# Performance work log

Hardware: AMD Instinct MI355X
Metric: run time of the kernel (lower is better)

## Reference

```python
import jax, jax.numpy as jnp
import numpy as np

B, N, K = 8, 2048, 32
EPS = 1e-5


def _lrelu(x):
    return jnp.where(x >= 0, x, 0.2 * x)


def _bn(x, p):
    # inference BatchNorm; x: [B, C, ...], p: [4, C] = (gamma, beta, mean, var)
    g, b, m, v = p[0], p[1], p[2], p[3]
    shape = (1, -1) + (1,) * (x.ndim - 2)
    scale = g * jax.lax.rsqrt(v + EPS)
    return (x - m.reshape(shape)) * scale.reshape(shape) + b.reshape(shape)


def _group(x, k):
    # ops.group with xyz_or_feature='feature', feature_or_diff='diff'
    # x: [B, C, N] -> edge features [B, 2C, N, k] = cat(neighbor - center, center)
    xt = jnp.transpose(x, (0, 2, 1))  # [B, N, C]
    sq = jnp.sum(xt * xt, axis=-1)    # [B, N]
    dist = sq[:, :, None] - 2.0 * jnp.einsum('bnc,bmc->bnm', xt, xt) + sq[:, None, :]
    idx = jax.lax.top_k(-dist, k)[1]  # [B, N, k] nearest neighbors
    nbr = jax.vmap(lambda f, i: f[i])(xt, idx)  # [B, N, k, C]
    center = xt[:, :, None, :]
    edge = jnp.concatenate([nbr - center, jnp.broadcast_to(center, nbr.shape)], axis=-1)
    return jnp.transpose(edge, (0, 3, 1, 2))  # [B, 2C, N, k]


def _edgeconv(x, w1, bn1, w2, bn2, k):
    e = _group(x, k)
    h = _lrelu(_bn(jnp.einsum('oc,bcnk->bonk', w1, e), bn1))
    h = _lrelu(_bn(jnp.einsum('oc,bcnk->bonk', w2, h), bn2))
    return jnp.max(h, axis=-1)  # max over neighbors -> [B, C_out, N]


def _model(x,
           ec1_w1, ec1_bn1, ec1_w2, ec1_bn2,
           ec2_w1, ec2_bn1, ec2_w2, ec2_bn2,
           ec3_w1, ec3_bn1, ec3_w2, ec3_bn2,
           emb_w, q_w, k_w, v_w, att_bn1, ff_w1, ff_w2, att_bn2,
           cb_w, cb_bn):
    # EdgeConvBlock (3 stacked EdgeConvs, outputs concatenated)
    f1 = _edgeconv(x, ec1_w1, ec1_bn1, ec1_w2, ec1_bn2, K)
    f2 = _edgeconv(f1, ec2_w1, ec2_bn1, ec2_w2, ec2_bn2, K)
    f3 = _edgeconv(f2, ec3_w1, ec3_bn1, ec3_w2, ec3_bn2, K)
    xc = jnp.concatenate([f1, f2, f3], axis=1)  # [B, 192, N]
    # Point2PointAttentionBlock: embedding then dense self-attention
    h = jnp.einsum('oc,bcn->bon', emb_w, xc)  # [B, 1024, N]
    q = jnp.einsum('oc,bcn->bon', q_w, h)
    kk = jnp.einsum('oc,bcn->bon', k_w, h)
    v = jnp.einsum('oc,bcn->bon', v_w, h)
    scale = jnp.sqrt(jnp.asarray(h.shape[1], h.dtype))
    att = jax.nn.softmax(jnp.einsum('bcn,bcm->bnm', q, kk) / scale, axis=-1)  # [B, N, N]
    x_r = jnp.einsum('bnm,bcm->bcn', att, v)
    h = _bn(h + x_r, att_bn1)
    ff = jnp.einsum('oc,bcn->bon', ff_w2, _lrelu(jnp.einsum('oc,bcn->bon', ff_w1, h)))
    h = _bn(h + ff, att_bn2)
    # ConvBlock head
    return _lrelu(_bn(jnp.einsum('oc,bcn->bon', cb_w, h), cb_bn))  # [B, 1024, N]


def setup_inputs() -> dict:
    key = jax.random.key(0)
    ks = iter(jax.random.split(key, 32))

    def randn(shape, s=0.1):
        return jax.random.normal(next(ks), shape, jnp.float32) * s

    def bnp(c):
        return jax.random.uniform(next(ks), (4, c), jnp.float32, 0.1, 1.0)

    return {
        'x': randn((B, 3, N), 1.0),
        'ec1_w1': randn((64, 6)), 'ec1_bn1': bnp(64),
        'ec1_w2': randn((64, 64)), 'ec1_bn2': bnp(64),
        'ec2_w1': randn((64, 128)), 'ec2_bn1': bnp(64),
        'ec2_w2': randn((64, 64)), 'ec2_bn2': bnp(64),
        'ec3_w1': randn((64, 128)), 'ec3_bn1': bnp(64),
        'ec3_w2': randn((64, 64)), 'ec3_bn2': bnp(64),
        'emb_w': randn((1024, 192), 0.05),
        'q_w': randn((1024, 1024), 0.03),
        'k_w': randn((1024, 1024), 0.03),
        'v_w': randn((1024, 1024), 0.03),
        'att_bn1': bnp(1024),
        'ff_w1': randn((512, 1024), 0.03),
        'ff_w2': randn((1024, 512), 0.03),
        'att_bn2': bnp(1024),
        'cb_w': randn((1024, 1024), 0.03),
        'cb_bn': bnp(1024),
    }


def reference(x,
              ec1_w1, ec1_bn1, ec1_w2, ec1_bn2,
              ec2_w1, ec2_bn1, ec2_w2, ec2_bn2,
              ec3_w1, ec3_bn1, ec3_w2, ec3_bn2,
              emb_w, q_w, k_w, v_w, att_bn1, ff_w1, ff_w2, att_bn2,
              cb_w, cb_bn):
    return _model(x,
                  ec1_w1, ec1_bn1, ec1_w2, ec1_bn2,
                  ec2_w1, ec2_bn1, ec2_w2, ec2_bn2,
                  ec3_w1, ec3_bn1, ec3_w2, ec3_bn2,
                  emb_w, q_w, k_w, v_w, att_bn1, ff_w1, ff_w2, att_bn2,
                  cb_w, cb_bn)
```

## Files before the change

kernel.cpp:

```cpp
#include <hip/hip_runtime.h>
#include <hip/hip_bf16.h>

constexpr int Bn  = 8;
constexpr int Np  = 2048;
constexpr int KNN = 32;

typedef __attribute__((ext_vector_type(8))) short bf16x8;
typedef __attribute__((ext_vector_type(4))) float f32x4;

__device__ static inline void gll16(const void* g, void* l) {
  __builtin_amdgcn_global_load_lds((const __attribute__((address_space(1))) void*)g,
                                   (__attribute__((address_space(3))) void*)l, 16, 0, 0);
}

__device__ static inline unsigned short f2bf(float x) {
  union { __hip_bfloat16 h; unsigned short u; } cv; cv.h = __float2bfloat16(x); return cv.u;
}
__device__ static inline float bf2f(unsigned short u) {
  union { __hip_bfloat16 h; unsigned short u; } cv; cv.u = u; return __bfloat162float(cv.h);
}

__global__ __launch_bounds__(256)
void cvt_bf16_kernel(const float* __restrict__ s, __hip_bfloat16* __restrict__ d, int n) {
  int i = blockIdx.x * 256 + threadIdx.x;
  if (i < n) d[i] = __float2bfloat16(s[i]);
}

template<int CIN, int K1>
__global__ __launch_bounds__(256)
void cvt_w1a(const float* __restrict__ w1, __hip_bfloat16* __restrict__ out) {
  int i = blockIdx.x * 256 + threadIdx.x;
  if (i >= 64 * K1) return;
  int o = i / K1, c = i - o * K1;
  out[i] = __float2bfloat16(c < CIN ? w1[o * 2 * CIN + c] : 0.f);
}

__global__ __launch_bounds__(256)
void xpose_kernel(const float* __restrict__ x, float* __restrict__ xt,
                  __hip_bfloat16* __restrict__ xb) {
  int i = blockIdx.x * 256 + threadIdx.x;
  int b = i >> 11, n = i & 2047;
  const float* p = x + (long)b * 3 * Np + n;
  float vx = p[0], vy = p[Np], vz = p[2 * Np];
  xt[(long)i * 4 + 0] = vx;
  xt[(long)i * 4 + 1] = vy;
  xt[(long)i * 4 + 2] = vz;
  xt[(long)i * 4 + 3] = 0.f;
  __hip_bfloat16* q = xb + (long)i * 8;
  q[0] = __float2bfloat16(vx); q[1] = __float2bfloat16(vy);
  q[2] = __float2bfloat16(vz);
  q[3] = __float2bfloat16(0.f); q[4] = q[3]; q[5] = q[3]; q[6] = q[3]; q[7] = q[3];
}

template<int C, int CP>
__global__ __launch_bounds__(256)
void sq_kernel(const float* __restrict__ f, float* __restrict__ out) {
  int i = blockIdx.x * 256 + threadIdx.x;
  const float* p = f + (long)i * CP;
  float s = 0.f;
#pragma unroll
  for (int c = 0; c < C; ++c) s += p[c] * p[c];
  out[i] = s;
}

template<int CIN, int CP>
__global__ __launch_bounds__(256)
void split_kernel(const float* __restrict__ f, __hip_bfloat16* __restrict__ fhi,
                  __hip_bfloat16* __restrict__ flo) {
  int i = blockIdx.x * 256 + threadIdx.x;
  int n = i >> 6, c = i & 63;
  float v = (c < CIN) ? f[(long)n * CP + c] : 0.f;
  __hip_bfloat16 h = __float2bfloat16(v);
  fhi[i] = h;
  flo[i] = __float2bfloat16(v - __bfloat162float(h));
}

__device__ static inline unsigned umin32(unsigned a, unsigned b) { return a < b ? a : b; }

__device__ static inline unsigned long long shfl64x(unsigned long long k, int m) {
  unsigned lo = (unsigned)__shfl_xor((int)(unsigned)k, m);
  unsigned hi = (unsigned)__shfl_xor((int)(unsigned)(k >> 32), m);
  return ((unsigned long long)hi << 32) | (unsigned long long)lo;
}

__device__ static inline unsigned lane_sort64_u32(unsigned v, int lane) {
#pragma unroll
  for (int k = 2; k <= 64; k <<= 1) {
#pragma unroll
    for (int j = k >> 1; j > 0; j >>= 1) {
      unsigned o = (unsigned)__shfl_xor((int)v, j);
      bool dir = ((lane & k) == 0);
      bool lower = ((lane & j) == 0);
      bool keep = (v < o) == (dir == lower);
      v = keep ? v : o;
    }
  }
  return v;
}

__device__ static inline unsigned long long lane_sort64_u64(unsigned long long v, int lane) {
#pragma unroll
  for (int k = 2; k <= 64; k <<= 1) {
#pragma unroll
    for (int j = k >> 1; j > 0; j >>= 1) {
      unsigned long long o = shfl64x(v, j);
      bool dir = ((lane & k) == 0);
      bool lower = ((lane & j) == 0);
      bool keep = (v < o) == (dir == lower);
      v = keep ? v : o;
    }
  }
  return v;
}

__device__ static inline unsigned long long lane_merge64(unsigned long long a,
                                                         unsigned long long b, int lane) {
  unsigned long long br = shfl64x(b, 63);
  unsigned long long m = a < br ? a : br;
#pragma unroll
  for (int j = 32; j > 0; j >>= 1) {
    unsigned long long o = shfl64x(m, j);
    bool lower = ((lane & j) == 0);
    bool keep = (m < o) == lower;
    m = keep ? m : o;
  }
  return m;
}

template<int MAP>
__device__ static inline void row_topk(const unsigned* val, unsigned long long* cbuf,
                                       int lane, int* outp) {
  unsigned tmn[16];
#pragma unroll
  for (int i = 0; i < 16; ++i) tmn[i] = umin32(val[i], val[i + 16]);
#pragma unroll
  for (int w2 = 8; w2 >= 1; w2 >>= 1)
#pragma unroll
    for (int i = 0; i < 8; ++i)
      if (i < w2) tmn[i] = umin32(tmn[i], tmn[i + w2]);

  unsigned T = (unsigned)__shfl((int)lane_sort64_u32(tmn[0], lane), 31);

  int S = 0;
#pragma unroll
  for (int s = 0; s < 32; ++s) {
    bool p = val[s] <= T;
    unsigned long long mask = __ballot(p);
    int pre = __builtin_amdgcn_mbcnt_hi((unsigned)(mask >> 32),
              __builtin_amdgcn_mbcnt_lo((unsigned)mask, 0u));
    int pos = S + pre;
    unsigned idx = (MAP == 0) ? (unsigned)((s >> 2) * 256 + lane * 4 + (s & 3))
                              : (unsigned)((s >> 2) * 256 + (s & 3) * 64 + lane);
    if (p && pos < 256) cbuf[pos] = ((unsigned long long)val[s] << 32) | idx;
    S += (int)__popcll(mask);
  }

  unsigned long long cur;
  if (S <= 256) {
    unsigned long long k0 = (lane < S) ? cbuf[lane] : ~0ull;
    cur = lane_sort64_u64(k0, lane);
    for (int c = 64; c < S; c += 64) {
      unsigned long long kc = (c + lane < S) ? cbuf[c + lane] : ~0ull;
      cur = lane_merge64(cur, lane_sort64_u64(kc, lane), lane);
    }
  } else {
    cur = ~0ull;
    for (int s = 0; s < 32; ++s) {
      unsigned idx = (MAP == 0) ? (unsigned)((s >> 2) * 256 + lane * 4 + (s & 3))
                                : (unsigned)((s >> 2) * 256 + (s & 3) * 64 + lane);
      unsigned long long kc = ((unsigned long long)val[s] << 32) | idx;
      cur = lane_merge64(cur, lane_sort64_u64(kc, lane), lane);
    }
  }
  if (lane < KNN) outp[lane] = (int)(unsigned)cur;
}

__global__ __launch_bounds__(512)
void knn3_kernel(const float* __restrict__ xt, const float* __restrict__ sqb,
                 int* __restrict__ idxOut) {
  __shared__ float4 F[2048];
  __shared__ float sqS[2048];
  __shared__ unsigned long long cbuf[8 * 256];
  int t = threadIdx.x, lane = t & 63, w = t >> 6;
  long pb = (long)blockIdx.y * Np;
  for (int e = t; e < 2048; e += 512) {
    F[e] = ((const float4*)xt)[pb + e];
    sqS[e] = sqb[pb + e];
  }
  __syncthreads();
  int row = blockIdx.x * 8 + w;
  float4 a = F[row];
  unsigned val[32];
#pragma unroll
  for (int j4 = 0; j4 < 8; ++j4)
#pragma unroll
    for (int u = 0; u < 4; ++u) {
      int col = j4 * 256 + u * 64 + lane;
      float4 fb = F[col];
      float d = sqS[col] - 2.f * (a.x * fb.x + a.y * fb.y + a.z * fb.z);
      unsigned b = __float_as_uint(d);
      val[j4 * 4 + u] = b ^ ((unsigned)((int)b >> 31) | 0x80000000u);
    }
  row_topk<1>(val, cbuf + w * 256, lane, idxOut + (pb + row) * KNN);
}

__global__ __launch_bounds__(512)
void knn16_kernel(const __hip_bfloat16* __restrict__ fhi,
                  const __hip_bfloat16* __restrict__ flo,
                  const float* __restrict__ sqb, int* __restrict__ idxOut) {
  constexpr int LDW = 2052;
  __shared__ __align__(16) float Dw[16 * LDW];
  __shared__ float sqS[2048];
  __shared__ unsigned long long cbuf[8 * 256];
  int t = threadIdx.x, lane = t & 63, w = t >> 6;
  long pb = (long)blockIdx.y * Np;
  int r0 = blockIdx.x * 16;
  const __hip_bfloat16* fh = fhi + pb * 64;
  const __hip_bfloat16* fl = flo + pb * 64;

  ((float4*)sqS)[t] = ((const float4*)(sqb + pb))[t];

  int ar = r0 + (lane & 15);
  int kc = (lane >> 4) * 8;
  bf16x8 ah[2], al[2];
#pragma unroll
  for (int k2 = 0; k2 < 2; ++k2) {
    ah[k2] = *(const bf16x8*)(fh + (long)ar * 64 + k2 * 32 + kc);
    al[k2] = *(const bf16x8*)(fl + (long)ar * 64 + k2 * 32 + kc);
  }
  __syncthreads();

  int cb0 = w * 256;
  bf16x8 bh[2], bl[2];
  {
    int bcol = cb0 + (lane & 15);
#pragma unroll
    for (int k2 = 0; k2 < 2; ++k2) {
      bh[k2] = *(const bf16x8*)(fh + (long)bcol * 64 + k2 * 32 + kc);
      bl[k2] = *(const bf16x8*)(fl + (long)bcol * 64 + k2 * 32 + kc);
    }
  }
  for (int ct = 0; ct < 16; ++ct) {
    bf16x8 nh[2], nl[2];
    if (ct < 15) {
      int bcol = cb0 + (ct + 1) * 16 + (lane & 15);
#pragma unroll
      for (int k2 = 0; k2 < 2; ++k2) {
        nh[k2] = *(const bf16x8*)(fh + (long)bcol * 64 + k2 * 32 + kc);
        nl[k2] = *(const bf16x8*)(fl + (long)bcol * 64 + k2 * 32 + kc);
      }
    }
    f32x4 acc = f32x4{0.f, 0.f, 0.f, 0.f};
#pragma unroll
    for (int k2 = 0; k2 < 2; ++k2) {
      acc = __builtin_amdgcn_mfma_f32_16x16x32_bf16(ah[k2], bh[k2], acc, 0, 0, 0);
      acc = __builtin_amdgcn_mfma_f32_16x16x32_bf16(ah[k2], bl[k2], acc, 0, 0, 0);
      acc = __builtin_amdgcn_mfma_f32_16x16x32_bf16(al[k2], bh[k2], acc, 0, 0, 0);
    }
    int col0 = cb0 + ct * 16;
    int n = lane & 15, m0 = (lane >> 4) * 4;
    float sqv = sqS[col0 + n];
#pragma unroll
    for (int r = 0; r < 4; ++r)
      Dw[(m0 + r) * LDW + col0 + n] = sqv - 2.f * acc[r];
#pragma unroll
    for (int k2 = 0; k2 < 2; ++k2) { bh[k2] = nh[k2]; bl[k2] = nl[k2]; }
  }
  __syncthreads();

  for (int rr = 0; rr < 2; ++rr) {
    int row = w * 2 + rr;
    unsigned val[32];
    const float4* rp = (const float4*)&Dw[row * LDW];
#pragma unroll
    for (int j4 = 0; j4 < 8; ++j4) {
      float4 f4 = rp[j4 * 64 + lane];
      float fv[4] = {f4.x, f4.y, f4.z, f4.w};
#pragma unroll
      for (int u = 0; u < 4; ++u) {
        unsigned b = __float_as_uint(fv[u]);
        val[j4 * 4 + u] = b ^ ((unsigned)((int)b >> 31) | 0x80000000u);
      }
    }
    row_topk<0>(val, cbuf + w * 256, lane, idxOut + (pb + r0 + row) * KNN);
  }
}

template<int CIN, int CP>
__global__ __launch_bounds__(256)
void biasker(const float* __restrict__ feat, const float* __restrict__ w1,
             float* __restrict__ bias) {
  __shared__ float wd[64][CIN + 1];
  int tid = threadIdx.x;
  for (int e = tid; e < 64 * CIN; e += 256) {
    int o = e / CIN, c = e - o * CIN;
    wd[o][c] = w1[o * 2 * CIN + CIN + c] - w1[o * 2 * CIN + c];
  }
  __syncthreads();
  int wv = tid >> 6, o = tid & 63;
  float wr_[CIN];
#pragma unroll
  for (int c = 0; c < CIN; ++c) wr_[c] = wd[o][c];
  long base = (long)blockIdx.y * Np + blockIdx.x * 32 + wv * 8;
  for (int p = 0; p < 8; ++p) {
    const float* fr = feat + (base + p) * CP;
    float acc = 0.f;
#pragma unroll
    for (int c = 0; c < CIN; ++c) acc = fmaf(wr_[c], fr[c], acc);
    bias[(base + p) * 64 + o] = acc;
  }
}

template<int K1>
__global__ __launch_bounds__(256)
void edge_mfma(const __hip_bfloat16* __restrict__ featb, int fstride,
               const int* __restrict__ idx, const float* __restrict__ bias,
               const __hip_bfloat16* __restrict__ w1b,
               const __hip_bfloat16* __restrict__ w2b,
               const float* __restrict__ bn1, const float* __restrict__ bn2,
               float* __restrict__ fout, __hip_bfloat16* __restrict__ xcseg) {
  __shared__ __align__(16) char lds[32768 + 64 * K1 * 2 + 8192 + 1024 + 512];
  __hip_bfloat16* A  = (__hip_bfloat16*)lds;
  __hip_bfloat16* H1 = A + 128 * K1;
  float*          H2 = (float*)lds;
  __hip_bfloat16* W1 = (__hip_bfloat16*)(lds + 32768);
  __hip_bfloat16* W2 = W1 + 64 * K1;
  float* biasS = (float*)(lds + 32768 + 64 * K1 * 2 + 8192);
  int*   idxS  = (int*)(biasS + 256);

  int t = threadIdx.x, lane = t & 63, w = t >> 6;
  long pb = (long)blockIdx.y * Np;
  int p0 = blockIdx.x * 4;

  if (t < 128) idxS[t] = idx[(pb + p0 + (t >> 5)) * KNN + (t & 31)];
  biasS[w * 64 + lane] = bias[(pb + p0 + w) * 64 + lane];
  for (int e = t; e < 64 * K1 / 8; e += 256)
    ((ulonglong2*)W1)[e] = ((const ulonglong2*)w1b)[e];
  for (int e = t; e < 512; e += 256)
    ((ulonglong2*)W2)[e] = ((const ulonglong2*)w2b)[e];
  __syncthreads();

  if (K1 == 64) {
#pragma unroll
    for (int i = 0; i < 4; ++i) {
      int e = t + i * 256;
      int r = e >> 3, cc = e & 7;
      const ulonglong2* src = (const ulonglong2*)(featb + (pb + idxS[r]) * fstride) + cc;
      ((ulonglong2*)(A + r * 64))[cc] = *src;
    }
  } else {
    if (t < 128) {
      int r = t;
      ulonglong2 z; z.x = 0; z.y = 0;
      ((ulonglong2*)(A + r * 32))[0] = *(const ulonglong2*)(featb + (pb + idxS[r]) * fstride);
      ((ulonglong2*)(A + r * 32))[1] = z;
      ((ulonglong2*)(A + r * 32))[2] = z;
      ((ulonglong2*)(A + r * 32))[3] = z;
    }
  }

  int ocol = lane & 15;
  float sc1[4], sh1[4], sc2[4], sh2[4];
#pragma unroll
  for (int jn = 0; jn < 4; ++jn) {
    int o = jn * 16 + ocol;
    sc1[jn] = bn1[o] * rsqrtf(bn1[192 + o] + 1e-5f);
    sh1[jn] = bn1[64 + o] - bn1[128 + o] * sc1[jn];
    sc2[jn] = bn2[o] * rsqrtf(bn2[192 + o] + 1e-5f);
    sh2[jn] = bn2[64 + o] - bn2[128 + o] * sc2[jn];
  }
  __syncthreads();

  int mrow = lane & 15;
  int kc   = (lane >> 4) * 8;
  constexpr int KS = K1 / 32;

  f32x4 acc[2][4];
#pragma unroll
  for (int im = 0; im < 2; ++im)
#pragma unroll
    for (int jn = 0; jn < 4; ++jn) acc[im][jn] = f32x4{0.f, 0.f, 0.f, 0.f};
#pragma unroll
  for (int s = 0; s < KS; ++s) {
    bf16x8 af[2], bf_[4];
#pragma unroll
    for (int im = 0; im < 2; ++im)
      af[im] = *(const bf16x8*)(A + (w * 32 + im * 16 + mrow) * K1 + s * 32 + kc);
#pragma unroll
    for (int jn = 0; jn < 4; ++jn)
      bf_[jn] = *(const bf16x8*)(W1 + (jn * 16 + mrow) * K1 + s * 32 + kc);
#pragma unroll
    for (int im = 0; im < 2; ++im)
#pragma unroll
      for (int jn = 0; jn < 4; ++jn)
        acc[im][jn] = __builtin_amdgcn_mfma_f32_16x16x32_bf16(af[im], bf_[jn], acc[im][jn], 0, 0, 0);
  }
#pragma unroll
  for (int im = 0; im < 2; ++im)
#pragma unroll
    for (int jn = 0; jn < 4; ++jn) {
      int o = jn * 16 + ocol;
      float bsv = biasS[w * 64 + o];
#pragma unroll
      for (int r = 0; r < 4; ++r) {
        int m = w * 32 + im * 16 + (lane >> 4) * 4 + r;
        float x = (acc[im][jn][r] + bsv) * sc1[jn] + sh1[jn];
        x = fmaxf(x, 0.2f * x);
        H1[m * 64 + o] = __float2bfloat16(x);
      }
    }
  __syncthreads();

  bf16x8 a2[2][2], b2[4][2];
#pragma unroll
  for (int im = 0; im < 2; ++im)
#pragma unroll
    for (int s = 0; s < 2; ++s)
      a2[im][s] = *(const bf16x8*)(H1 + (w * 32 + im * 16 + mrow) * 64 + s * 32 + kc);
#pragma unroll
  for (int jn = 0; jn < 4; ++jn)
#pragma unroll
    for (int s = 0; s < 2; ++s)
      b2[jn][s] = *(const bf16x8*)(W2 + (jn * 16 + mrow) * 64 + s * 32 + kc);
  __syncthreads();

  f32x4 acc2[2][4];
#pragma unroll
  for (int im = 0; im < 2; ++im)
#pragma unroll
    for (int jn = 0; jn < 4; ++jn) acc2[im][jn] = f32x4{0.f, 0.f, 0.f, 0.f};
#pragma unroll
  for (int s = 0; s < 2; ++s)
#pragma unroll
    for (int im = 0; im < 2; ++im)
#pragma unroll
      for (int jn = 0; jn < 4; ++jn)
        acc2[im][jn] = __builtin_amdgcn_mfma_f32_16x16x32_bf16(a2[im][s], b2[jn][s], acc2[im][jn], 0, 0, 0);
#pragma unroll
  for (int im = 0; im < 2; ++im)
#pragma unroll
    for (int jn = 0; jn < 4; ++jn) {
      int o = jn * 16 + ocol;
#pragma unroll
      for (int r = 0; r < 4; ++r) {
        int m = w * 32 + im * 16 + (lane >> 4) * 4 + r;
        float x = acc2[im][jn][r] * sc2[jn] + sh2[jn];
        x = fmaxf(x, 0.2f * x);
        H2[m * 64 + o] = x;
      }
    }
  __syncthreads();

  {
    int o = t & 63;
    float m = -3.4e38f;
#pragma unroll
    for (int k = 0; k < 32; ++k) m = fmaxf(m, H2[(w * 32 + k) * 64 + o]);
    int n2 = p0 + w;
    if (fout) fout[(pb + n2) * 64 + o] = m;
    xcseg[(pb + n2) * 192 + o] = __float2bfloat16(m);
  }
}

template<int OUTF, int BNMODE, int RESID, int LRELU>
__global__ __launch_bounds__(512)
void gemm_db(const __hip_bfloat16* __restrict__ A, int lda, long sA,
             const __hip_bfloat16* __restrict__ B, int ldb, long sB,
             void* __restrict__ Cv, int ldc, long sC,
             const __hip_bfloat16* __restrict__ R, long sR,
             const float* __restrict__ bn, int bnlen, int Kd,
             int gx, int gy) {
  int nwg = gx * gy * Bn;
  int cpx = nwg >> 3;
  int orig = blockIdx.x;
  int wg = (orig & 7) * cpx + (orig >> 3);
  int bz = wg / (gx * gy);
  int rem = wg - bz * (gx * gy);
  int by = rem / gx;
  int bx = rem - by * gx;
  A += (long)bz * sA;
  B += (long)bz * sB;
  long i0 = (long)bx * 256, j0 = (long)by * 256;

  __shared__ __hip_bfloat16 As[2][256 * 64];
  __shared__ __hip_bfloat16 Bs[2][256 * 64];

  int t = threadIdx.x, lane = t & 63, w = t >> 6;
  int wm = w & 1, wn = w >> 1;

  f32x4 acc[8][4];
#pragma unroll
  for (int im = 0; im < 8; ++im)
#pragma unroll
    for (int jn = 0; jn < 4; ++jn) acc[im][jn] = f32x4{0.f, 0.f, 0.f, 0.f};

#define STAGE_DB(bi, kt)                                                     \
  {                                                                          \
    _Pragma("unroll")                                                        \
    for (int i = 0; i < 4; ++i) {                                            \
      int e = t + i * 512;                                                   \
      int r = e >> 3, c = e & 7;                                             \
      int cs = c ^ (r & 7);                                                  \
      gll16(A + (i0 + r) * lda + (kt) * 64 + cs * 8,                         \
            (__hip_bfloat16*)As[bi] + e * 8);                                \
    }                                                                        \
    _Pragma("unroll")                                                        \
    for (int i = 0; i < 4; ++i) {                                            \
      int e = t + i * 512;                                                   \
      int r = e >> 3, c = e & 7;                                             \
      int cs = c ^ (r & 7);                                                  \
      gll16(B + (j0 + r) * ldb + (kt) * 64 + cs * 8,                         \
            (__hip_bfloat16*)Bs[bi] + e * 8);                                \
    }                                                                        \
  }

  int nt = Kd >> 6;
  STAGE_DB(0, 0);
  __syncthreads();

  int cur = 0;
  for (int kt = 0; kt < nt; ++kt) {
    if (kt + 1 < nt) STAGE_DB(cur ^ 1, kt + 1);
    const __hip_bfloat16* Ab = As[cur];
    const __hip_bfloat16* Bb = Bs[cur];
#pragma unroll
    for (int ks = 0; ks < 2; ++ks) {
      bf16x8 af[8], bfv[4];
#pragma unroll
      for (int im = 0; im < 8; ++im) {
        int ra = wm * 128 + im * 16 + (lane & 15);
        int q = (ks * 4 + (lane >> 4)) ^ (ra & 7);
        af[im] = *(const bf16x8*)(Ab + ra * 64 + q * 8);
      }
#pragma unroll
      for (int jn = 0; jn < 4; ++jn) {
        int rb = wn * 64 + jn * 16 + (lane & 15);
        int q = (ks * 4 + (lane >> 4)) ^ (rb & 7);
        bfv[jn] = *(const bf16x8*)(Bb + rb * 64 + q * 8);
      }
#pragma unroll
      for (int im = 0; im < 8; ++im)
#pragma unroll
        for (int jn = 0; jn < 4; ++jn)
          acc[im][jn] = __builtin_amdgcn_mfma_f32_16x16x32_bf16(af[im], bfv[jn], acc[im][jn], 0, 0, 0);
    }
    __syncthreads();
    cur ^= 1;
  }
#undef STAGE_DB

  int mlocal = (lane >> 4) * 4;
  int nlocal = lane & 15;
#pragma unroll
  for (int i = 0; i < 8; ++i) {
    long m0 = i0 + wm * 128 + i * 16 + mlocal;
    float bsc[4], bsh[4];
    if (BNMODE == 1) {
#pragma unroll
      for (int r = 0; r < 4; ++r) {
        long c = m0 + r;
        float sc = bn[c] * rsqrtf(bn[3 * bnlen + c] + 1e-5f);
        bsc[r] = sc;
        bsh[r] = bn[bnlen + c] - bn[2 * bnlen + c] * sc;
      }
    }
#pragma unroll
    for (int j = 0; j < 4; ++j) {
      long nn = j0 + wn * 64 + j * 16 + nlocal;
      float sc2 = 1.f, sh2 = 0.f;
      if (BNMODE == 2) {
        sc2 = bn[nn] * rsqrtf(bn[3 * bnlen + nn] + 1e-5f);
        sh2 = bn[bnlen + nn] - bn[2 * bnlen + nn] * sc2;
      }
      f32x4 v = acc[i][j];
      float o4[4];
      ushort4 rv;
      if (RESID) rv = *(const ushort4*)(R + (long)bz * sR + nn * ldc + m0);
#pragma unroll
      for (int r = 0; r < 4; ++r) {
        float x = v[r];
        if (RESID) x += bf2f(r == 0 ? rv.x : r == 1 ? rv.y : r == 2 ? rv.z : rv.w);
        if (BNMODE == 1) x = x * bsc[r] + bsh[r];
        if (BNMODE == 2) x = x * sc2 + sh2;
        if (LRELU) x = (x >= 0.f) ? x : 0.2f * x;
        o4[r] = x;
      }
      if (OUTF) {
        float* Cp = (float*)Cv + (long)bz * sC + nn * ldc + m0;
        *(float4*)Cp = make_float4(o4[0], o4[1], o4[2], o4[3]);
      } else {
        __hip_bfloat16* Cp = (__hip_bfloat16*)Cv + (long)bz * sC + nn * ldc + m0;
        ushort4 sv;
        sv.x = f2bf(o4[0]); sv.y = f2bf(o4[1]); sv.z = f2bf(o4[2]); sv.w = f2bf(o4[3]);
        *(ushort4*)Cp = sv;
      }
    }
  }
}

__global__ __launch_bounds__(256)
void softmax_bf(__hip_bfloat16* __restrict__ S) {
  long row = (long)blockIdx.y * Np + blockIdx.x;
  __hip_bfloat16* p = S + row * Np;
  int t = threadIdx.x;
  const float scale = 0.03125f;
  float v[8];
  float mx = -3.4e38f;
#pragma unroll
  for (int u = 0; u < 8; ++u) {
    v[u] = __bfloat162float(p[u * 256 + t]) * scale;
    mx = fmaxf(mx, v[u]);
  }
  __shared__ float red[4];
#pragma unroll
  for (int off = 32; off > 0; off >>= 1) mx = fmaxf(mx, __shfl_xor(mx, off));
  if ((t & 63) == 0) red[t >> 6] = mx;
  __syncthreads();
  mx = fmaxf(fmaxf(red[0], red[1]), fmaxf(red[2], red[3]));
  __syncthreads();
  float sum = 0.f;
#pragma unroll
  for (int u = 0; u < 8; ++u) { v[u] = __expf(v[u] - mx); sum += v[u]; }
#pragma unroll
  for (int off = 32; off > 0; off >>= 1) sum += __shfl_xor(sum, off);
  if ((t & 63) == 0) red[t >> 6] = sum;
  __syncthreads();
  sum = red[0] + red[1] + red[2] + red[3];
  float inv = 1.f / sum;
#pragma unroll
  for (int u = 0; u < 8; ++u) p[u * 256 + t] = __float2bfloat16(v[u] * inv);
}

extern "C" void kernel_launch(void* const* d_in, const int* in_sizes, int n_in,
                              void* d_out, int out_size, void* d_ws, size_t ws_size,
                              hipStream_t stream) {
  const float* x       = (const float*)d_in[0];
  const float* ec1_w1  = (const float*)d_in[1];
  const float* ec1_bn1 = (const float*)d_in[2];
  const float* ec1_w2  = (const float*)d_in[3];
  const float* ec1_bn2 = (const float*)d_in[4];
  const float* ec2_w1  = (const float*)d_in[5];
  const float* ec2_bn1 = (const float*)d_in[6];
  const float* ec2_w2  = (const float*)d_in[7];
  const float* ec2_bn2 = (const float*)d_in[8];
  const float* ec3_w1  = (const float*)d_in[9];
  const float* ec3_bn1 = (const float*)d_in[10];
  const float* ec3_w2  = (const float*)d_in[11];
  const float* ec3_bn2 = (const float*)d_in[12];
  const float* emb_w   = (const float*)d_in[13];
  const float* q_w     = (const float*)d_in[14];
  const float* k_w     = (const float*)d_in[15];
  const float* v_w     = (const float*)d_in[16];
  const float* att_bn1 = (const float*)d_in[17];
  const float* ff_w1   = (const float*)d_in[18];
  const float* ff_w2   = (const float*)d_in[19];
  const float* att_bn2 = (const float*)d_in[20];
  const float* cb_w    = (const float*)d_in[21];
  const float* cb_bn   = (const float*)d_in[22];
  float* out = (float*)d_out;
  (void)in_sizes; (void)n_in; (void)out_size; (void)ws_size;

  float* ws  = (float*)d_ws;
  float* xt  = ws;
  float* f1  = xt + 65536;
  float* f2  = f1 + 1048576;
  float* sqb = f2 + 1048576;
  int*   idxb = (int*)(sqb + 16384);
  __hip_bfloat16* xc  = (__hip_bfloat16*)(idxb + 524288);
  __hip_bfloat16* wts = xc + 3145728;
  __hip_bfloat16* ew  = wts + 5439488;
  __hip_bfloat16* xb  = ew + 22528;
  float* big = (float*)(xb + 131072);
  __hip_bfloat16* hb  = (__hip_bfloat16*)big;
  __hip_bfloat16* qb  = hb + 16777216;
  __hip_bfloat16* kb  = qb + 16777216;
  __hip_bfloat16* vtb = kb + 16777216;
  __hip_bfloat16* Sb  = vtb + 16777216;
  __hip_bfloat16* fhi = (__hip_bfloat16*)big;
  __hip_bfloat16* flo = fhi + 1048576;
  float* biasb = big + 33554432;

  __hip_bfloat16* emb_wb = wts;
  __hip_bfloat16* q_wb   = wts + 196608;
  __hip_bfloat16* k_wb   = wts + 1245184;
  __hip_bfloat16* v_wb   = wts + 2293760;
  __hip_bfloat16* ff1_wb = wts + 3342336;
  __hip_bfloat16* ff2_wb = wts + 3866624;
  __hip_bfloat16* cb_wb  = wts + 4390912;

  __hip_bfloat16* w1a1_b = ew;
  __hip_bfloat16* w2_1b  = ew + 2048;
  __hip_bfloat16* w1a2_b = ew + 6144;
  __hip_bfloat16* w2_2b  = ew + 10240;
  __hip_bfloat16* w1a3_b = ew + 14336;
  __hip_bfloat16* w2_3b  = ew + 18432;

  const long sN1024 = (long)Np * 1024;
  const long sN512  = (long)Np * 512;
  const long sN192  = (long)Np * 192;
  const long sNN    = (long)Np * Np;

  cvt_bf16_kernel<<<768,  256, 0, stream>>>(emb_w, emb_wb, 196608);
  cvt_bf16_kernel<<<4096, 256, 0, stream>>>(q_w,   q_wb,   1048576);
  cvt_bf16_kernel<<<4096, 256, 0, stream>>>(k_w,   k_wb,   1048576);
  cvt_bf16_kernel<<<4096, 256, 0, stream>>>(v_w,   v_wb,   1048576);
  cvt_bf16_kernel<<<2048, 256, 0, stream>>>(ff_w1, ff1_wb, 524288);
  cvt_bf16_kernel<<<2048, 256, 0, stream>>>(ff_w2, ff2_wb, 524288);
  cvt_bf16_kernel<<<4096, 256, 0, stream>>>(cb_w,  cb_wb,  1048576);
  cvt_w1a<3, 32><<<8, 256, 0, stream>>>(ec1_w1, w1a1_b);
  cvt_w1a<64, 64><<<16, 256, 0, stream>>>(ec2_w1, w1a2_b);
  cvt_w1a<64, 64><<<16, 256, 0, stream>>>(ec3_w1, w1a3_b);
  cvt_bf16_kernel<<<16, 256, 0, stream>>>(ec1_w2, w2_1b, 4096);
  cvt_bf16_kernel<<<16, 256, 0, stream>>>(ec2_w2, w2_2b, 4096);
  cvt_bf16_kernel<<<16, 256, 0, stream>>>(ec3_w2, w2_3b, 4096);

  xpose_kernel<<<64, 256, 0, stream>>>(x, xt, xb);

  sq_kernel<3, 4><<<64, 256, 0, stream>>>(xt, sqb);
  knn3_kernel<<<dim3(Np / 8, Bn), 512, 0, stream>>>(xt, sqb, idxb);
  biasker<3, 4><<<dim3(Np / 32, Bn), 256, 0, stream>>>(xt, ec1_w1, biasb);
  edge_mfma<32><<<dim3(Np / 4, Bn), 256, 0, stream>>>(
      xb, 8, idxb, biasb, w1a1_b, w2_1b, ec1_bn1, ec1_bn2, f1, xc);

  sq_kernel<64, 64><<<64, 256, 0, stream>>>(f1, sqb);
  split_kernel<64, 64><<<4096, 256, 0, stream>>>(f1, fhi, flo);
  knn16_kernel<<<dim3(Np / 16, Bn), 512, 0, stream>>>(fhi, flo, sqb, idxb);
  biasker<64, 64><<<dim3(Np / 32, Bn), 256, 0, stream>>>(f1, ec2_w1, biasb);
  edge_mfma<64><<<dim3(Np / 4, Bn), 256, 0, stream>>>(
      xc, 192, idxb, biasb, w1a2_b, w2_2b, ec2_bn1, ec2_bn2, f2, xc + 64);

  sq_kernel<64, 64><<<64, 256, 0, stream>>>(f2, sqb);
  split_kernel<64, 64><<<4096, 256, 0, stream>>>(f2, fhi, flo);
  knn16_kernel<<<dim3(Np / 16, Bn), 512, 0, stream>>>(fhi, flo, sqb, idxb);
  biasker<64, 64><<<dim3(Np / 32, Bn), 256, 0, stream>>>(f2, ec3_w1, biasb);
  edge_mfma<64><<<dim3(Np / 4, Bn), 256, 0, stream>>>(
      xc + 64, 192, idxb, biasb, w1a3_b, w2_3b, ec3_bn1, ec3_bn2, nullptr, xc + 128);

  gemm_db<0, 0, 0, 0><<<dim3(4 * 8 * Bn), 512, 0, stream>>>(
      emb_wb, 192, 0, xc, 192, sN192, hb, 1024, sN1024, nullptr, 0, nullptr, 0, 192, 4, 8);

  gemm_db<0, 0, 0, 0><<<dim3(4 * 8 * Bn), 512, 0, stream>>>(
      q_wb, 1024, 0, hb, 1024, sN1024, qb, 1024, sN1024, nullptr, 0, nullptr, 0, 1024, 4, 8);
  gemm_db<0, 0, 0, 0><<<dim3(4 * 8 * Bn), 512, 0, stream>>>(
      k_wb, 1024, 0, hb, 1024, sN1024, kb, 1024, sN1024, nullptr, 0, nullptr, 0, 1024, 4, 8);
  gemm_db<0, 0, 0, 0><<<dim3(8 * 4 * Bn), 512, 0, stream>>>(
      hb, 1024, sN1024, v_wb, 1024, 0, vtb, 2048, sN1024, nullptr, 0, nullptr, 0, 1024, 8, 4);

  gemm_db<0, 0, 0, 0><<<dim3(8 * 8 * Bn), 512, 0, stream>>>(
      kb, 1024, sN1024, qb, 1024, sN1024, Sb, 2048, sNN, nullptr, 0, nullptr, 0, 1024, 8, 8);
  softmax_bf<<<dim3(Np, Bn), 256, 0, stream>>>(Sb);

  gemm_db<0, 1, 1, 0><<<dim3(4 * 8 * Bn), 512, 0, stream>>>(
      vtb, 2048, sN1024, Sb, 2048, sNN, hb, 1024, sN1024, hb, sN1024, att_bn1, 1024, 2048, 4, 8);

  gemm_db<0, 0, 0, 1><<<dim3(2 * 8 * Bn), 512, 0, stream>>>(
      ff1_wb, 1024, 0, hb, 1024, sN1024, qb, 512, sN512, nullptr, 0, nullptr, 0, 1024, 2, 8);
  gemm_db<0, 1, 1, 0><<<dim3(4 * 8 * Bn), 512, 0, stream>>>(
      ff2_wb, 512, 0, qb, 512, sN512, hb, 1024, sN1024, hb, sN1024, att_bn2, 1024, 512, 4, 8);

  gemm_db<1, 2, 0, 1><<<dim3(8 * 4 * Bn), 512, 0, stream>>>(
      hb, 1024, sN1024, cb_wb, 1024, 0, out, 2048, sN1024, nullptr, 0, cb_bn, 1024, 1024, 8, 4);
}
```

Before: 952.6 us.

## Shrink knn16 tile to 8 rows to cut LDS and raise occupancy

The 64-channel kNN kernel now handles 8 query rows per block instead of 16. That shrinks the distance tile in shared memory, drops the staged squared-norm array in favour of direct global loads, and caps the candidate buffer at 224 entries. Two column-tile streams are interleaved with software prefetch, and launch bounds ask for 4 blocks per CU. The MFMA still computes 16 rows, so half of each product is wasted work, and B-operand loads are repeated across twice as many blocks. A row with more than 224 candidates now takes the slower full-merge path more often.

```diff
diff --git a/kernel.cpp b/kernel.cpp
--- a/kernel.cpp
+++ b/kernel.cpp
@@ -127,7 +127,7 @@
   return m;
 }
 
-template<int MAP>
+template<int MAP, int CAP>
 __device__ static inline void row_topk(const unsigned* val, unsigned long long* cbuf,
                                        int lane, int* outp) {
   unsigned tmn[16];
@@ -151,12 +151,12 @@
     int pos = S + pre;
     unsigned idx = (MAP == 0) ? (unsigned)((s >> 2) * 256 + lane * 4 + (s & 3))
                               : (unsigned)((s >> 2) * 256 + (s & 3) * 64 + lane);
-    if (p && pos < 256) cbuf[pos] = ((unsigned long long)val[s] << 32) | idx;
+    if (p && pos < CAP) cbuf[pos] = ((unsigned long long)val[s] << 32) | idx;
     S += (int)__popcll(mask);
   }
 
   unsigned long long cur;
-  if (S <= 256) {
+  if (S <= CAP) {
     unsigned long long k0 = (lane < S) ? cbuf[lane] : ~0ull;
     cur = lane_sort64_u64(k0, lane);
     for (int c = 64; c < S; c += 64) {
@@ -201,77 +201,121 @@
       unsigned b = __float_as_uint(d);
       val[j4 * 4 + u] = b ^ ((unsigned)((int)b >> 31) | 0x80000000u);
     }
-  row_topk<1>(val, cbuf + w * 256, lane, idxOut + (pb + row) * KNN);
-}
-
-__global__ __launch_bounds__(512)
+  row_topk<1, 256>(val, cbuf + w * 256, lane, idxOut + (pb + row) * KNN);
+}
+
+__global__ __launch_bounds__(512, 4)
 void knn16_kernel(const __hip_bfloat16* __restrict__ fhi,
                   const __hip_bfloat16* __restrict__ flo,
                   const float* __restrict__ sqb, int* __restrict__ idxOut) {
   constexpr int LDW = 2052;
-  __shared__ __align__(16) float Dw[16 * LDW];
-  __shared__ float sqS[2048];
-  __shared__ unsigned long long cbuf[8 * 256];
+  constexpr int CAP = 224;
+  __shared__ __align__(16) float Dw[8 * LDW];
+  __shared__ unsigned long long cbuf[8 * CAP];
   int t = threadIdx.x, lane = t & 63, w = t >> 6;
   long pb = (long)blockIdx.y * Np;
-  int r0 = blockIdx.x * 16;
+  int r0 = blockIdx.x * 8;
   const __hip_bfloat16* fh = fhi + pb * 64;
   const __hip_bfloat16* fl = flo + pb * 64;
-
-  ((float4*)sqS)[t] = ((const float4*)(sqb + pb))[t];
-
-  int ar = r0 + (lane & 15);
+  const float* sqg = sqb + pb;
+
+  int ar = r0 + (lane & 7);
   int kc = (lane >> 4) * 8;
+  int n15 = lane & 15;
   bf16x8 ah[2], al[2];
 #pragma unroll
   for (int k2 = 0; k2 < 2; ++k2) {
     ah[k2] = *(const bf16x8*)(fh + (long)ar * 64 + k2 * 32 + kc);
     al[k2] = *(const bf16x8*)(fl + (long)ar * 64 + k2 * 32 + kc);
   }
-  __syncthreads();
 
   int cb0 = w * 256;
-  bf16x8 bh[2], bl[2];
+  bf16x8 b0h[2], b0l[2], b1h[2], b1l[2];
+  float sq0, sq1;
   {
-    int bcol = cb0 + (lane & 15);
+    int bc = cb0 + n15;
 #pragma unroll
     for (int k2 = 0; k2 < 2; ++k2) {
-      bh[k2] = *(const bf16x8*)(fh + (long)bcol * 64 + k2 * 32 + kc);
-      bl[k2] = *(const bf16x8*)(fl + (long)bcol * 64 + k2 * 32 + kc);
-    }
-  }
-  for (int ct = 0; ct < 16; ++ct) {
-    bf16x8 nh[2], nl[2];
-    if (ct < 15) {
-      int bcol = cb0 + (ct + 1) * 16 + (lane & 15);
+      b0h[k2] = *(const bf16x8*)(fh + (long)bc * 64 + k2 * 32 + kc);
+      b0l[k2] = *(const bf16x8*)(fl + (long)bc * 64 + k2 * 32 + kc);
+    }
+    sq0 = sqg[bc];
+    bc = cb0 + 16 + n15;
+#pragma unroll
+    for (int k2 = 0; k2 < 2; ++k2) {
+      b1h[k2] = *(const bf16x8*)(fh + (long)bc * 64 + k2 * 32 + kc);
+      b1l[k2] = *(const bf16x8*)(fl + (long)bc * 64 + k2 * 32 + kc);
+    }
+    sq1 = sqg[bc];
+  }
+  int m0 = (lane >> 4) * 4;
+  bool wr = (lane < 32);
+#pragma unroll
+  for (int cp = 0; cp < 8; ++cp) {
+    {
+      int ct = cp * 2;
+      bf16x8 nh[2], nl[2]; float nsq = 0.f;
+      if (ct + 2 < 16) {
+        int bc = cb0 + (ct + 2) * 16 + n15;
+#pragma unroll
+        for (int k2 = 0; k2 < 2; ++k2) {
+          nh[k2] = *(const bf16x8*)(fh + (long)bc * 64 + k2 * 32 + kc);
+          nl[k2] = *(const bf16x8*)(fl + (long)bc * 64 + k2 * 32 + kc);
+        }
+        nsq = sqg[bc];
+      }
+      f32x4 acc = f32x4{0.f, 0.f, 0.f, 0.f};
 #pragma unroll
       for (int k2 = 0; k2 < 2; ++k2) {
-        nh[k2] = *(const bf16x8*)(fh + (long)bcol * 64 + k2 * 32 + kc);
-        nl[k2] = *(const bf16x8*)(fl + (long)bcol * 64 + k2 * 32 + kc);
-      }
-    }
-    f32x4 acc = f32x4{0.f, 0.f, 0.f, 0.f};
-#pragma unroll
-    for (int k2 = 0; k2 < 2; ++k2) {
-      acc = __builtin_amdgcn_mfma_f32_16x16x32_bf16(ah[k2], bh[k2], acc, 0, 0, 0);
-      acc = __builtin_amdgcn_mfma_f32_16x16x32_bf16(ah[k2], bl[k2], acc, 0, 0, 0);
-      acc = __builtin_amdgcn_mfma_f32_16x16x32_bf16(al[k2], bh[k2], acc, 0, 0, 0);
-    }
-    int col0 = cb0 + ct * 16;
-    int n = lane & 15, m0 = (lane >> 4) * 4;
-    float sqv = sqS[col0 + n];
-#pragma unroll
-    for (int r = 0; r < 4; ++r)
-      Dw[(m0 + r) * LDW + col0 + n] = sqv - 2.f * acc[r];
-#pragma unroll
-    for (int k2 = 0; k2 < 2; ++k2) { bh[k2] = nh[k2]; bl[k2] = nl[k2]; }
-  }
-  __syncthreads();
-
-  for (int rr = 0; rr < 2; ++rr) {
-    int row = w * 2 + rr;
+        acc = __builtin_amdgcn_mfma_f32_16x16x32_bf16(ah[k2], b0h[k2], acc, 0, 0, 0);
+        acc = __builtin_amdgcn_mfma_f32_16x16x32_bf16(ah[k2], b0l[k2], acc, 0, 0, 0);
+        acc = __builtin_amdgcn_mfma_f32_16x16x32_bf16(al[k2], b0h[k2], acc, 0, 0, 0);
+      }
+      if (wr) {
+        int col = cb0 + ct * 16 + n15;
+#pragma unroll
+        for (int r = 0; r < 4; ++r)
+          Dw[(m0 + r) * LDW + col] = sq0 - 2.f * acc[r];
+      }
+#pragma unroll
+      for (int k2 = 0; k2 < 2; ++k2) { b0h[k2] = nh[k2]; b0l[k2] = nl[k2]; }
+      sq0 = nsq;
+    }
+    {
+      int ct = cp * 2 + 1;
+      bf16x8 nh[2], nl[2]; float nsq = 0.f;
+      if (ct + 2 < 16) {
+        int bc = cb0 + (ct + 2) * 16 + n15;
+#pragma unroll
+        for (int k2 = 0; k2 < 2; ++k2) {
+          nh[k2] = *(const bf16x8*)(fh + (long)bc * 64 + k2 * 32 + kc);
+          nl[k2] = *(const bf16x8*)(fl + (long)bc * 64 + k2 * 32 + kc);
+        }
+        nsq = sqg[bc];
+      }
+      f32x4 acc = f32x4{0.f, 0.f, 0.f, 0.f};
+#pragma unroll
+      for (int k2 = 0; k2 < 2; ++k2) {
+        acc = __builtin_amdgcn_mfma_f32_16x16x32_bf16(ah[k2], b1h[k2], acc, 0, 0, 0);
+        acc = __builtin_amdgcn_mfma_f32_16x16x32_bf16(ah[k2], b1l[k2], acc, 0, 0, 0);
+        acc = __builtin_amdgcn_mfma_f32_16x16x32_bf16(al[k2], b1h[k2], acc, 0, 0, 0);
+      }
+      if (wr) {
+        int col = cb0 + ct * 16 + n15;
+#pragma unroll
+        for (int r = 0; r < 4; ++r)
+          Dw[(m0 + r) * LDW + col] = sq1 - 2.f * acc[r];
+      }
+#pragma unroll
+      for (int k2 = 0; k2 < 2; ++k2) { b1h[k2] = nh[k2]; b1l[k2] = nl[k2]; }
+      sq1 = nsq;
+    }
+  }
+  __syncthreads();
+
+  {
     unsigned val[32];
-    const float4* rp = (const float4*)&Dw[row * LDW];
+    const float4* rp = (const float4*)&Dw[w * LDW];
 #pragma unroll
     for (int j4 = 0; j4 < 8; ++j4) {
       float4 f4 = rp[j4 * 64 + lane];
@@ -282,7 +326,7 @@
         val[j4 * 4 + u] = b ^ ((unsigned)((int)b >> 31) | 0x80000000u);
       }
     }
-    row_topk<0>(val, cbuf + w * 256, lane, idxOut + (pb + r0 + row) * KNN);
+    row_topk<0, CAP>(val, cbuf + w * CAP, lane, idxOut + (pb + r0 + w) * KNN);
   }
 }
 
@@ -724,14 +768,14 @@
 
   sq_kernel<64, 64><<<64, 256, 0, stream>>>(f1, sqb);
   split_kernel<64, 64><<<4096, 256, 0, stream>>>(f1, fhi, flo);
-  knn16_kernel<<<dim3(Np / 16, Bn), 512, 0, stream>>>(fhi, flo, sqb, idxb);
+  knn16_kernel<<<dim3(Np / 8, Bn), 512, 0, stream>>>(fhi, flo, sqb, idxb);
   biasker<64, 64><<<dim3(Np / 32, Bn), 256, 0, stream>>>(f1, ec2_w1, biasb);
   edge_mfma<64><<<dim3(Np / 4, Bn), 256, 0, stream>>>(
       xc, 192, idxb, biasb, w1a2_b, w2_2b, ec2_bn1, ec2_bn2, f2, xc + 64);
 
   sq_kernel<64, 64><<<64, 256, 0, stream>>>(f2, sqb);
   split_kernel<64, 64><<<4096, 256, 0, stream>>>(f2, fhi, flo);
-  knn16_kernel<<<dim3(Np / 16, Bn), 512, 0, stream>>>(fhi, flo, sqb, idxb);
+  knn16_kernel<<<dim3(Np / 8, Bn), 512, 0, stream>>>(fhi, flo, sqb, idxb);
   biasker<64, 64><<<dim3(Np / 32, Bn), 256, 0, stream>>>(f2, ec3_w1, biasb);
   edge_mfma<64><<<dim3(Np / 4, Bn), 256, 0, stream>>>(
       xc + 64, 192, idxb, biasb, w1a3_b, w2_3b, ec3_bn1, ec3_bn2, nullptr, xc + 128);
```

Result: slower. 1.012 ms (+6.3%).
